# Kernel optimization log

Hardware: AMD Instinct MI355X
Metric: run time of the kernel (lower is better)

The kernel has to match this reference:

```python
import jax, jax.numpy as jnp
import numpy as np

C = 256
K = C // 2  # inter_channels


def setup_inputs() -> dict:
    key = jax.random.key(0)
    ks = jax.random.split(key, 9)
    B, H, W = 8, 64, 64
    x = jax.random.normal(ks[0], (B, C, H, W), dtype=jnp.float32)
    def lin(k, out_c, in_c, scale):
        return jax.random.normal(k, (out_c, in_c), dtype=jnp.float32) * scale
    s_in = 1.0 / np.sqrt(C)
    s_k = 1.0 / np.sqrt(K)
    return {
        "x": x,
        "theta_w": lin(ks[1], K, C, s_in), "theta_b": jnp.zeros((K,), jnp.float32),
        "phi_w":   lin(ks[2], K, C, s_in), "phi_b":   jnp.zeros((K,), jnp.float32),
        "g_w":     lin(ks[3], K, C, s_in), "g_b":     jnp.zeros((K,), jnp.float32),
        "out_w":   lin(ks[4], C, K, s_k),  "out_b":   jnp.zeros((C,), jnp.float32),
    }


def reference(x, theta_w, theta_b, phi_w, phi_b, g_w, g_b, out_w, out_b):
    B, Cc, H, W = x.shape
    N = H * W
    xf = x.reshape(B, Cc, N)  # [B, C, N]
    # 1x1 convs == per-pixel linear projections
    theta = jnp.einsum('bcn,kc->bnk', xf, theta_w) + theta_b            # [B, N, K]
    phi   = jnp.einsum('bcn,kc->bkn', xf, phi_w) + phi_b[:, None]       # [B, K, N]
    g     = jnp.einsum('bcn,kc->bnk', xf, g_w) + g_b                    # [B, N, K]
    attn = jax.nn.softmax(jnp.einsum('bnk,bkm->bnm', theta, phi), axis=-1)  # [B, N, N]
    y = jnp.einsum('bnm,bmk->bnk', attn, g)                             # [B, N, K]
    out = jnp.einsum('bnk,ck->bcn', y, out_w) + out_b[:, None]          # [B, C, N]
    return out.reshape(B, Cc, H, W) + x
```

## Files before the change

kernel.cpp:

```cpp
#include <hip/hip_runtime.h>

typedef __attribute__((ext_vector_type(8))) _Float16 f16x8;
typedef __attribute__((ext_vector_type(4))) float f32x4;
typedef __attribute__((ext_vector_type(16))) float f32x16;
typedef __attribute__((ext_vector_type(2))) int int2v;
typedef __attribute__((ext_vector_type(4))) int int4v;

#define DEVI __device__ __forceinline__

DEVI unsigned short f2h(float f){
  _Float16 h = (_Float16)f;
  return __builtin_bit_cast(unsigned short, h);
}
DEVI float fexp2(float x){ return __builtin_amdgcn_exp2f(x); }

__global__ __launch_bounds__(256) void k_wconv(
    const float* __restrict__ tw, const float* __restrict__ pw,
    const float* __restrict__ gw, const float* __restrict__ ow,
    unsigned short* __restrict__ dst){
  int i = blockIdx.x*256 + threadIdx.x;
  int a = i>>15, off = i & 32767;
  const float* s = (a==0)?tw:(a==1)?pw:(a==2)?gw:ow;
  dst[i] = f2h(s[off]);
}

__global__ __launch_bounds__(256) void k_proj(
    const float* __restrict__ x,
    const unsigned short* __restrict__ Wq, const unsigned short* __restrict__ Wk,
    const unsigned short* __restrict__ Wg,
    const float* __restrict__ tb, const float* __restrict__ pb,
    const float* __restrict__ gb,
    unsigned short* __restrict__ Q, unsigned short* __restrict__ Km,
    unsigned short* __restrict__ VT)
{
  __shared__ __align__(16) unsigned short xT[64*264];
  const int tid = threadIdx.x;
  const int w = tid>>6, l = tid&63, l15 = l&15, lhi = l>>4;
  const int id = blockIdx.x;
  const int b = id & 7, n0 = (id>>3)*64;

  const float* xb = x + (size_t)b*256*4096 + n0;
  #pragma unroll 4
  for (int i=0;i<32;++i){
    int c = 64*w + 2*i;
    float v0 = xb[(size_t)c*4096 + l];
    float v1 = xb[(size_t)(c+1)*4096 + l];
    unsigned int pk = (unsigned int)f2h(v0) | ((unsigned int)f2h(v1)<<16);
    *(unsigned int*)&xT[l*264 + c] = pk;
  }
  __syncthreads();

  for (int mat=0; mat<2; ++mat){
    const unsigned short* Wm = mat ? Wk : Wq;
    const float* bias = mat ? pb : tb;
    unsigned short* Out = mat ? Km : Q;
    const float scl = mat ? 1.0f : 1.44269504f;
    for (int pbk=0; pbk<4; ++pbk){
      f16x8 aF[8];
      #pragma unroll
      for (int ks=0;ks<8;++ks)
        aF[ks] = *(const f16x8*)&xT[(16*pbk + l15)*264 + lhi*8 + 32*ks];
      #pragma unroll
      for (int kb2=0; kb2<2; ++kb2){
        int kb = 2*w + kb2;
        f32x4 acc = {0.f,0.f,0.f,0.f};
        #pragma unroll
        for (int ks=0;ks<8;++ks){
          f16x8 bF = *(const f16x8*)&Wm[(size_t)(16*kb + l15)*256 + lhi*8 + 32*ks];
          acc = __builtin_amdgcn_mfma_f32_16x16x32_f16(aF[ks], bF, acc, 0,0,0);
        }
        float bv = bias[16*kb + l15];
        #pragma unroll
        for (int r=0;r<4;++r){
          int pix = 16*pbk + lhi*4 + r;
          Out[((size_t)b*4096 + n0 + pix)*128 + 16*kb + l15] = f2h((acc[r] + bv)*scl);
        }
      }
    }
  }

  for (int nb=0; nb<4; ++nb){
    f16x8 bF[8];
    #pragma unroll
    for (int ks=0;ks<8;++ks)
      bF[ks] = *(const f16x8*)&xT[(16*nb + l15)*264 + lhi*8 + 32*ks];
    #pragma unroll
    for (int mb2=0; mb2<2; ++mb2){
      int mb = 2*w + mb2;
      f32x4 acc = {0.f,0.f,0.f,0.f};
      #pragma unroll
      for (int ks=0;ks<8;++ks){
        f16x8 aF = *(const f16x8*)&Wg[(size_t)(16*mb + l15)*256 + lhi*8 + 32*ks];
        acc = __builtin_amdgcn_mfma_f32_16x16x32_f16(aF, bF[ks], acc, 0,0,0);
      }
      #pragma unroll
      for (int r=0;r<4;++r){
        int k = 16*mb + lhi*4 + r;
        VT[((size_t)b*128 + k)*4096 + n0 + 16*nb + l15] = f2h(acc[r] + gb[k]);
      }
    }
  }
}

DEVI void stage_tiles(const char* Kg, const char* Vg, int nt,
                      char* Kd, char* Vd, int w, int l){
  #pragma unroll
  for (int c=0;c<4;++c){
    int base = (4*w + c)*1024;
    int lin  = base + l*16;
    int row = lin>>8, colb = lin&255;
    int f = ((row&7) ^ ((row>>2)&4)) << 4;
    const char* g = Kg + (size_t)(nt*64 + row)*256 + (colb ^ f);
    __builtin_amdgcn_global_load_lds((const __attribute__((address_space(1))) void*)g,
        (__attribute__((address_space(3))) void*)(Kd + base), 16, 0, 0);
  }
  #pragma unroll
  for (int c=0;c<4;++c){
    int base = (4*w + c)*1024;
    int lin  = base + l*16;
    int row = lin>>7, colb = lin&127;
    int f = ((row&7) ^ ((row>>2)&4)) << 4;
    const char* g = Vg + (size_t)row*8192 + (size_t)nt*128 + (colb ^ f);
    __builtin_amdgcn_global_load_lds((const __attribute__((address_space(1))) void*)g,
        (__attribute__((address_space(3))) void*)(Vd + base), 16, 0, 0);
  }
}

__global__ __launch_bounds__(256, 2) void k_attn(
    const unsigned short* __restrict__ Q, const unsigned short* __restrict__ Km,
    const unsigned short* __restrict__ VT,
    unsigned short* __restrict__ On,
    float* __restrict__ Mp, float* __restrict__ Lp)
{
  __shared__ __align__(16) unsigned short K_lds[2][64*128];
  __shared__ __align__(16) unsigned short V_lds[2][128*64];
  const int tid = threadIdx.x;
  const int w = tid>>6, l = tid&63;
  const int q32 = l & 31, hi = l >> 5;
  const int id = blockIdx.x;
  const int b = id & 7;
  const int qt = (id >> 3) & 31, h = id >> 8;
  const int n0 = qt*128, wq0 = w*32, nt0 = h*32;
  const int swz = ((q32&7) ^ ((q32>>2)&4)) << 4;

  const unsigned short* Qrow = Q + ((size_t)b*4096 + n0 + wq0 + q32)*128;
  f16x8 qf[8];
  #pragma unroll
  for (int ks=0; ks<8; ++ks)
    qf[ks] = *(const f16x8*)&Qrow[ks*16 + hi*8];

  const char* Kg = (const char*)(Km + (size_t)b*4096*128);
  const char* Vg = (const char*)(VT + (size_t)b*128*4096);

  float m_run = -3.0e38f, l_run = 0.f;
  f32x16 ob[4] = {};

  stage_tiles(Kg, Vg, nt0, (char*)K_lds[0], (char*)V_lds[0], w, l);
  __syncthreads();

  for (int it=0; it<32; ++it){
    const int cur = it & 1;
    if (it+1 < 32)
      stage_tiles(Kg, Vg, nt0+it+1, (char*)K_lds[cur^1], (char*)V_lds[cur^1], w, l);

    const char* Kc = (const char*)K_lds[cur];
    f32x16 st[2];
    #pragma unroll
    for (int mt=0; mt<2; ++mt){
      f32x16 a = {};
      int rb = (32*mt + q32)*256;
      #pragma unroll
      for (int ks=0; ks<8; ++ks){
        f16x8 kf = *(const f16x8*)(Kc + rb + ((16*hi + 32*ks) ^ swz));
        a = __builtin_amdgcn_mfma_f32_32x32x16_f16(kf, qf[ks], a, 0,0,0);
      }
      st[mt] = a;
    }

    const char* Vc = (const char*)V_lds[cur];
    f16x8 vreg[16];
    #pragma unroll
    for (int ks=0; ks<4; ++ks)
      #pragma unroll
      for (int db=0; db<4; ++db)
        vreg[4*ks+db] = *(const f16x8*)(Vc + (32*db + q32)*128 + ((16*hi + 32*ks) ^ swz));

    float mx;
    {
      float t0 = fmaxf(fmaxf(st[0][0], st[0][1]), fmaxf(st[0][2], st[0][3]));
      float t1 = fmaxf(fmaxf(st[0][4], st[0][5]), fmaxf(st[0][6], st[0][7]));
      float t2 = fmaxf(fmaxf(st[0][8], st[0][9]), fmaxf(st[0][10], st[0][11]));
      float t3 = fmaxf(fmaxf(st[0][12], st[0][13]), fmaxf(st[0][14], st[0][15]));
      float t4 = fmaxf(fmaxf(st[1][0], st[1][1]), fmaxf(st[1][2], st[1][3]));
      float t5 = fmaxf(fmaxf(st[1][4], st[1][5]), fmaxf(st[1][6], st[1][7]));
      float t6 = fmaxf(fmaxf(st[1][8], st[1][9]), fmaxf(st[1][10], st[1][11]));
      float t7 = fmaxf(fmaxf(st[1][12], st[1][13]), fmaxf(st[1][14], st[1][15]));
      mx = fmaxf(fmaxf(fmaxf(t0,t1), fmaxf(t2,t3)), fmaxf(fmaxf(t4,t5), fmaxf(t6,t7)));
    }
    mx = fmaxf(mx, __shfl_xor(mx, 32));
    if (!__all(mx <= m_run + 11.5416f)){
      float mn = fmaxf(m_run, mx);
      float sc = fexp2(m_run - mn);
      l_run *= sc;
      #pragma unroll
      for (int db=0; db<4; ++db) ob[db] *= sc;
      m_run = mn;
    }
    float ps = 0.f;
    #pragma unroll
    for (int mt=0; mt<2; ++mt)
      #pragma unroll
      for (int r=0; r<16; ++r){
        float p = fexp2(st[mt][r] - m_run);
        st[mt][r] = p; ps += p;
      }
    l_run += ps + __shfl_xor(ps, 32);

    #pragma unroll
    for (int ks=0; ks<4; ++ks){
      const int mt = ks>>1, u = ks&1;
      int X0 = __builtin_bit_cast(int, __builtin_amdgcn_cvt_pkrtz(st[mt][8*u+0], st[mt][8*u+1]));
      int X1 = __builtin_bit_cast(int, __builtin_amdgcn_cvt_pkrtz(st[mt][8*u+2], st[mt][8*u+3]));
      int Y0 = __builtin_bit_cast(int, __builtin_amdgcn_cvt_pkrtz(st[mt][8*u+4], st[mt][8*u+5]));
      int Y1 = __builtin_bit_cast(int, __builtin_amdgcn_cvt_pkrtz(st[mt][8*u+6], st[mt][8*u+7]));
      int2v rA = __builtin_amdgcn_permlane32_swap(X0, Y0, false, false);
      int2v rB = __builtin_amdgcn_permlane32_swap(X1, Y1, false, false);
      int4v wv = {rA[0], rB[0], rA[1], rB[1]};
      f16x8 pf = __builtin_bit_cast(f16x8, wv);
      #pragma unroll
      for (int db=0; db<4; ++db)
        ob[db] = __builtin_amdgcn_mfma_f32_32x32x16_f16(vreg[4*ks+db], pf, ob[db], 0,0,0);
    }
    __syncthreads();
  }

  float invl = 1.0f / l_run;
  unsigned short* Orow = On + (((size_t)(h*8 + b)*4096) + n0 + wq0 + q32)*128;
  #pragma unroll
  for (int db=0; db<4; ++db)
    #pragma unroll
    for (int g=0; g<4; ++g){
      int2v pk2;
      pk2[0] = __builtin_bit_cast(int, __builtin_amdgcn_cvt_pkrtz(ob[db][4*g+0]*invl, ob[db][4*g+1]*invl));
      pk2[1] = __builtin_bit_cast(int, __builtin_amdgcn_cvt_pkrtz(ob[db][4*g+2]*invl, ob[db][4*g+3]*invl));
      *(int2v*)&Orow[32*db + 8*g + 4*hi] = pk2;
    }
  if (l < 32){
    size_t idx = (size_t)(h*8+b)*4096 + n0 + wq0 + l;
    Mp[idx] = m_run;
    Lp[idx] = l_run;
  }
}

__global__ __launch_bounds__(256) void k_merge(
    const unsigned short* __restrict__ On, const float* __restrict__ Mp,
    const float* __restrict__ Lp,
    const unsigned short* __restrict__ Wo, const float* __restrict__ out_b,
    const float* __restrict__ x, float* __restrict__ out)
{
  __shared__ __align__(16) unsigned short y_lds[32*136];
  const int tid = threadIdx.x;
  const int id = blockIdx.x;
  const int b = id & 7, n0 = (id>>3)*32;

  {
    int row = tid>>3, dq = (tid&7)*16;
    size_t i0 = (size_t)b*4096 + n0 + row;
    size_t i1 = (size_t)(8+b)*4096 + n0 + row;
    float m0 = Mp[i0], m1 = Mp[i1], l0 = Lp[i0], l1 = Lp[i1];
    float M = fmaxf(m0, m1);
    float a0 = fexp2(m0 - M)*l0, a1 = fexp2(m1 - M)*l1;
    float inv = 1.0f/(a0 + a1);
    float w0 = a0*inv, w1 = a1*inv;
    const unsigned short* p0 = On + i0*128 + dq;
    const unsigned short* p1 = On + i1*128 + dq;
    #pragma unroll
    for (int i=0;i<2;++i){
      f16x8 o0 = *(const f16x8*)&p0[8*i];
      f16x8 o1 = *(const f16x8*)&p1[8*i];
      int4v pk;
      #pragma unroll
      for (int j=0;j<4;++j){
        float ya = w0*(float)o0[2*j]   + w1*(float)o1[2*j];
        float yb = w0*(float)o0[2*j+1] + w1*(float)o1[2*j+1];
        pk[j] = __builtin_bit_cast(int, __builtin_amdgcn_cvt_pkrtz(ya, yb));
      }
      *(int4v*)&y_lds[row*136 + dq + 8*i] = pk;
    }
  }
  __syncthreads();

  const int w = tid>>6, l = tid&63, l15 = l&15, lhi = l>>4;
  const float* xb = x + (size_t)b*256*4096;
  const f32x4 zero4 = {0.f,0.f,0.f,0.f};
  for (int cb=0; cb<4; ++cb){
    int c0 = 64*w + 16*cb;
    f16x8 aW[4];
    #pragma unroll
    for (int ks=0;ks<4;++ks)
      aW[ks] = *(const f16x8*)&Wo[(size_t)(c0 + l15)*128 + lhi*8 + 32*ks];
    float obv[4];
    #pragma unroll
    for (int r=0;r<4;++r) obv[r] = out_b[c0 + lhi*4 + r];
    #pragma unroll
    for (int nb=0;nb<2;++nb){
      f32x4 acc = zero4;
      #pragma unroll
      for (int ks=0;ks<4;++ks){
        f16x8 yF = *(const f16x8*)&y_lds[(16*nb + l15)*136 + lhi*8 + 32*ks];
        acc = __builtin_amdgcn_mfma_f32_16x16x32_f16(aW[ks], yF, acc, 0,0,0);
      }
      #pragma unroll
      for (int r=0;r<4;++r){
        int c = c0 + lhi*4 + r;
        size_t oi = (size_t)c*4096 + n0 + 16*nb + l15;
        out[(size_t)b*256*4096 + oi] = acc[r] + obv[r] + xb[oi];
      }
    }
  }
}

extern "C" void kernel_launch(void* const* d_in, const int* in_sizes, int n_in,
                              void* d_out, int out_size, void* d_ws, size_t ws_size,
                              hipStream_t stream) {
  (void)in_sizes; (void)n_in; (void)out_size; (void)ws_size;
  const float* x  = (const float*)d_in[0];
  const float* tw = (const float*)d_in[1];
  const float* tb = (const float*)d_in[2];
  const float* pw = (const float*)d_in[3];
  const float* pb = (const float*)d_in[4];
  const float* gw = (const float*)d_in[5];
  const float* gb = (const float*)d_in[6];
  const float* ow = (const float*)d_in[7];
  const float* ob = (const float*)d_in[8];
  float* out = (float*)d_out;

  unsigned short* ws = (unsigned short*)d_ws;
  unsigned short* Wq = ws;
  unsigned short* Wk = ws + 32768;
  unsigned short* Wg = ws + 65536;
  unsigned short* Wo = ws + 98304;
  unsigned short* Q  = ws + 131072;
  unsigned short* Km = Q  + 4194304;
  unsigned short* VT = Km + 4194304;
  unsigned short* On = VT + 4194304;
  float* Mp = (float*)(On + 8388608);
  float* Lp = Mp + 65536;

  hipLaunchKernelGGL(k_wconv, dim3(512), dim3(256), 0, stream, tw, pw, gw, ow, ws);
  hipLaunchKernelGGL(k_proj,  dim3(512), dim3(256), 0, stream,
                     x, Wq, Wk, Wg, tb, pb, gb, Q, Km, VT);
  hipLaunchKernelGGL(k_attn,  dim3(512), dim3(256), 0, stream,
                     Q, Km, VT, On, Mp, Lp);
  hipLaunchKernelGGL(k_merge, dim3(1024), dim3(256), 0, stream,
                     On, Mp, Lp, Wo, ob, x, out);
}
```

Measured before the change: 131.5 us.

## Software-pipeline QK^T one tile ahead of softmax-PV with triple-buffered V

Restructures the attention loop so the QK^T MFMAs for tile t+1 are issued alongside the softmax and PV work for tile t, with V tiles triple-buffered in LDS. V fragments are now read from LDS inside the PV loop instead of being preloaded into registers. The row-sum cross-half shuffle is deferred to the end. This aims to overlap MFMA with exp/softmax VALU work, at the cost of more LDS (which may reduce occupancy from two blocks per CU) and higher register pressure from two live score sets.

```diff
diff --git a/kernel.cpp b/kernel.cpp
--- a/kernel.cpp
+++ b/kernel.cpp
@@ -102,8 +102,7 @@
   }
 }
 
-DEVI void stage_tiles(const char* Kg, const char* Vg, int nt,
-                      char* Kd, char* Vd, int w, int l){
+DEVI void stage_K(const char* Kg, int nt, char* Kd, int w, int l){
   #pragma unroll
   for (int c=0;c<4;++c){
     int base = (4*w + c)*1024;
@@ -114,6 +113,8 @@
     __builtin_amdgcn_global_load_lds((const __attribute__((address_space(1))) void*)g,
         (__attribute__((address_space(3))) void*)(Kd + base), 16, 0, 0);
   }
+}
+DEVI void stage_V(const char* Vg, int nt, char* Vd, int w, int l){
   #pragma unroll
   for (int c=0;c<4;++c){
     int base = (4*w + c)*1024;
@@ -133,7 +134,7 @@
     float* __restrict__ Mp, float* __restrict__ Lp)
 {
   __shared__ __align__(16) unsigned short K_lds[2][64*128];
-  __shared__ __align__(16) unsigned short V_lds[2][128*64];
+  __shared__ __align__(16) unsigned short V_lds[3][128*64];
   const int tid = threadIdx.x;
   const int w = tid>>6, l = tid&63;
   const int q32 = l & 31, hi = l >> 5;
@@ -152,19 +153,11 @@
   const char* Kg = (const char*)(Km + (size_t)b*4096*128);
   const char* Vg = (const char*)(VT + (size_t)b*128*4096);
 
-  float m_run = -3.0e38f, l_run = 0.f;
+  float m_run = -3.0e38f, l_loc = 0.f;
   f32x16 ob[4] = {};
-
-  stage_tiles(Kg, Vg, nt0, (char*)K_lds[0], (char*)V_lds[0], w, l);
-  __syncthreads();
-
-  for (int it=0; it<32; ++it){
-    const int cur = it & 1;
-    if (it+1 < 32)
-      stage_tiles(Kg, Vg, nt0+it+1, (char*)K_lds[cur^1], (char*)V_lds[cur^1], w, l);
-
-    const char* Kc = (const char*)K_lds[cur];
-    f32x16 st[2];
+  f32x16 stA[2], stB[2];
+
+  auto QKT = [&](const char* Kc, f32x16* st){
     #pragma unroll
     for (int mt=0; mt<2; ++mt){
       f32x16 a = {};
@@ -176,15 +169,9 @@
       }
       st[mt] = a;
     }
-
-    const char* Vc = (const char*)V_lds[cur];
-    f16x8 vreg[16];
-    #pragma unroll
-    for (int ks=0; ks<4; ++ks)
-      #pragma unroll
-      for (int db=0; db<4; ++db)
-        vreg[4*ks+db] = *(const f16x8*)(Vc + (32*db + q32)*128 + ((16*hi + 32*ks) ^ swz));
-
+  };
+
+  auto SMPV = [&](f32x16* st, const char* Vc){
     float mx;
     {
       float t0 = fmaxf(fmaxf(st[0][0], st[0][1]), fmaxf(st[0][2], st[0][3]));
@@ -201,7 +188,7 @@
     if (!__all(mx <= m_run + 11.5416f)){
       float mn = fmaxf(m_run, mx);
       float sc = fexp2(m_run - mn);
-      l_run *= sc;
+      l_loc *= sc;
       #pragma unroll
       for (int db=0; db<4; ++db) ob[db] *= sc;
       m_run = mn;
@@ -214,8 +201,7 @@
         float p = fexp2(st[mt][r] - m_run);
         st[mt][r] = p; ps += p;
       }
-    l_run += ps + __shfl_xor(ps, 32);
-
+    l_loc += ps;
     #pragma unroll
     for (int ks=0; ks<4; ++ks){
       const int mt = ks>>1, u = ks&1;
@@ -228,12 +214,49 @@
       int4v wv = {rA[0], rB[0], rA[1], rB[1]};
       f16x8 pf = __builtin_bit_cast(f16x8, wv);
       #pragma unroll
-      for (int db=0; db<4; ++db)
-        ob[db] = __builtin_amdgcn_mfma_f32_32x32x16_f16(vreg[4*ks+db], pf, ob[db], 0,0,0);
-    }
+      for (int db=0; db<4; ++db){
+        f16x8 vf = *(const f16x8*)(Vc + (32*db + q32)*128 + ((16*hi + 32*ks) ^ swz));
+        ob[db] = __builtin_amdgcn_mfma_f32_32x32x16_f16(vf, pf, ob[db], 0,0,0);
+      }
+    }
+  };
+
+  char* vprev = (char*)V_lds[2];
+  char* vcur  = (char*)V_lds[0];
+  char* vnext = (char*)V_lds[1];
+
+  stage_K(Kg, nt0, (char*)K_lds[0], w, l);
+  stage_V(Vg, nt0, vcur, w, l);
+  __syncthreads();
+
+  stage_K(Kg, nt0+1, (char*)K_lds[1], w, l);
+  stage_V(Vg, nt0+1, vnext, w, l);
+  QKT((const char*)K_lds[0], stA);
+  __syncthreads();
+  { char* t=vprev; vprev=vcur; vcur=vnext; vnext=t; }
+
+  #pragma unroll 1
+  for (int tt=0; tt<15; ++tt){
+    const int t1 = 2*tt+1;
+    stage_K(Kg, nt0+t1+1, (char*)K_lds[0], w, l);
+    stage_V(Vg, nt0+t1+1, vnext, w, l);
+    QKT((const char*)K_lds[1], stB);
+    SMPV(stA, vprev);
     __syncthreads();
-  }
-
+    { char* t=vprev; vprev=vcur; vcur=vnext; vnext=t; }
+    stage_K(Kg, nt0+t1+2, (char*)K_lds[1], w, l);
+    stage_V(Vg, nt0+t1+2, vnext, w, l);
+    QKT((const char*)K_lds[0], stA);
+    SMPV(stB, vprev);
+    __syncthreads();
+    { char* t=vprev; vprev=vcur; vcur=vnext; vnext=t; }
+  }
+  QKT((const char*)K_lds[1], stB);
+  SMPV(stA, vprev);
+  { char* t=vprev; vprev=vcur; vcur=vnext; vnext=t; }
+  SMPV(stB, vprev);
+
+  float l_run = l_loc + __shfl_xor(l_loc, 32);
   float invl = 1.0f / l_run;
   unsigned short* Orow = On + (((size_t)(h*8 + b)*4096) + n0 + wq0 + q32)*128;
   #pragma unroll
```

Result: no change. 129.1 us (-1.8%).
